# Kernel optimization log

Measured on AMD Instinct MI355X. Metric: run time of the kernel, lower is better.

Reference implementation:

```python
import jax, jax.numpy as jnp
import numpy as np

EPS = 1e-12  # torch F.normalize clamp_min eps


def _linear_interp(t, M):
    # PyTorch F.interpolate(mode='linear', align_corners=False) along last axis.
    L = t.shape[-1]
    src = (jnp.arange(M, dtype=t.dtype) + 0.5) * (L / M) - 0.5
    src = jnp.maximum(src, 0.0)
    i0 = jnp.minimum(jnp.floor(src).astype(jnp.int32), L - 1)
    i1 = jnp.minimum(i0 + 1, L - 1)
    frac = src - i0.astype(t.dtype)
    return t[..., i0] * (1.0 - frac) + t[..., i1] * frac


def _l2norm(t):
    n = jnp.linalg.norm(t, axis=-1, keepdims=True)
    return t / jnp.maximum(n, EPS)


def setup_inputs() -> dict:
    key = jax.random.key(0)
    ks = jax.random.split(key, 6)
    b, dim, m = 4, 512, 4096
    h = w = 64
    heads = 8
    s = 0.02
    return {
        "x": jax.random.normal(ks[0], (b, dim, m), dtype=jnp.float32),
        "y": jax.random.normal(ks[1], (b, dim, h, w), dtype=jnp.float32),
        "temperature": jnp.ones((heads, 1, 1), dtype=jnp.float32),
        "w_kv": jax.random.normal(ks[2], (2 * dim, dim), dtype=jnp.float32) * s,
        "w_q": jax.random.normal(ks[3], (dim, dim), dtype=jnp.float32) * s,
        "w_dw": jax.random.normal(ks[4], (dim, dim, 3, 3), dtype=jnp.float32) * s,
        "w_out": jax.random.normal(ks[5], (dim, dim), dtype=jnp.float32) * s,
    }


def reference(x, y, temperature, w_kv, w_q, w_dw, w_out):
    b, c, m = x.shape
    heads = temperature.shape[0]
    hd = c // heads

    # kv = Conv1d(dim, 2*dim, k=1)(x); split into k, v
    kv = jnp.einsum('bcm,oc->bom', x, w_kv)
    k, v = jnp.split(kv, 2, axis=1)

    # q = dwconv3x3(Conv2d 1x1(y)) -> flatten -> linear-resize to m
    q = jnp.einsum('bchw,oc->bohw', y, w_q)
    q = jax.lax.conv_general_dilated(
        q, w_dw, window_strides=(1, 1), padding=[(1, 1), (1, 1)],
        dimension_numbers=('NCHW', 'OIHW', 'NCHW'))
    q = q.reshape(b, c, -1)
    q = _linear_interp(q, m)

    # split heads: [b, head, c', m]
    q = _l2norm(q.reshape(b, heads, hd, m))
    k = _l2norm(k.reshape(b, heads, hd, m))
    v = v.reshape(b, heads, hd, m)

    # channel-wise attention: [b, head, c', c']
    attn = jnp.einsum('bhcm,bhdm->bhcd', q, k) * temperature
    attn = jax.nn.softmax(attn, axis=-1)
    out = jnp.einsum('bhcd,bhdm->bhcm', attn, v).reshape(b, c, m)

    # project_out: Conv1d k=1
    return jnp.einsum('bcm,oc->bom', out, w_out)
```

## Files before the change

kernel.cpp:

```cpp
#include <hip/hip_runtime.h>
#include <hip/hip_bf16.h>
#include <math.h>

typedef float f32x4 __attribute__((ext_vector_type(4)));
typedef int   i32x4 __attribute__((ext_vector_type(4)));
typedef short s16x8 __attribute__((ext_vector_type(8)));

#define NB 4
#define NC 512
#define NM 4096
#define NHEADS 8

#define GLDS16(src, dst) __builtin_amdgcn_global_load_lds( \
    (const __attribute__((address_space(1))) void*)(src),  \
    (__attribute__((address_space(3))) void*)(dst), 16, 0, 0)

__global__ __launch_bounds__(256) void prep(
    const float* __restrict__ wdw, const float* __restrict__ wkv,
    const float* __restrict__ wq,
    __hip_bfloat16* __restrict__ Wr, __hip_bfloat16* __restrict__ wkvB,
    __hip_bfloat16* __restrict__ wqT, __hip_bfloat16* __restrict__ zeropad,
    float* __restrict__ norms)
{
  long idx = (long)blockIdx.x * 256 + threadIdx.x;
  if (idx < 2359296) {
    int r = (int)(idx / 262144);
    int rem = (int)(idx % 262144);
    int o = rem >> 9, i = rem & 511;
    Wr[idx] = __float2bfloat16(wdw[((long)o * 512 + i) * 9 + r]);
  } else if (idx < 2883584) {
    long j = idx - 2359296;
    wkvB[j] = __float2bfloat16(wkv[j]);
  } else if (idx < 3145728) {
    long j = idx - 2883584;
    int c = (int)(j >> 9), cp = (int)(j & 511);
    wqT[j] = __float2bfloat16(wq[(long)cp * 512 + c]);
  } else if (idx < 3145856) {
    zeropad[idx - 3145728] = __float2bfloat16(0.f);
  } else if (idx < 3149952) {
    norms[idx - 3145856] = 0.f;
  }
}

__global__ __launch_bounds__(256) void transpose_k(
    const float* __restrict__ x, const float* __restrict__ y,
    __hip_bfloat16* __restrict__ xT, __hip_bfloat16* __restrict__ yT)
{
  __shared__ __hip_bfloat16 tile[64][68];
  int z = blockIdx.z;
  const float* src = ((z < 4) ? x : y) + (long)(z & 3) * ((long)NC * NM);
  __hip_bfloat16* dst = (z < 4 ? xT : yT) + (long)(z & 3) * ((long)NC * NM);
  int tm = blockIdx.x * 64, tc = blockIdx.y * 64;
  int tx4 = threadIdx.x & 15, trow = threadIdx.x >> 4;
  #pragma unroll
  for (int p = 0; p < 4; p++) {
    int crow = trow + p * 16;
    f32x4 v = *(const f32x4*)&src[(long)(tc + crow) * NM + tm + tx4 * 4];
    #pragma unroll
    for (int t = 0; t < 4; t++) tile[crow][tx4 * 4 + t] = __float2bfloat16(v[t]);
  }
  __syncthreads();
  #pragma unroll
  for (int p = 0; p < 4; p++) {
    int mrow = trow + p * 16;
    union { ushort4 u4; unsigned short u[4]; } o;
    #pragma unroll
    for (int t = 0; t < 4; t++)
      o.u[t] = *(const unsigned short*)&tile[tx4 * 4 + t][mrow];
    *(ushort4*)&dst[(long)(tm + mrow) * NC + tc + tx4 * 4] = o.u4;
  }
}

__global__ __launch_bounds__(256) void gemm_bt(
    const __hip_bfloat16* __restrict__ Aall, long sA,
    const __hip_bfloat16* __restrict__ Ball, long sB,
    __hip_bfloat16* __restrict__ Cball, float* __restrict__ Cfall, long sC,
    int M, int N, int Kd, int outF32)
{
  const __hip_bfloat16* A = Aall + (long)blockIdx.z * sA;
  const __hip_bfloat16* B = Ball + (long)blockIdx.z * sB;
  const int m0 = blockIdx.y * 128, n0 = blockIdx.x * 128;
  __shared__ __hip_bfloat16 As[128 * 32];
  __shared__ __hip_bfloat16 Bs[128 * 32];
  const int tid = threadIdx.x;
  const int wid = tid >> 6, lane = tid & 63;
  const int wm = (wid >> 1) * 64, wn = (wid & 1) * 64;
  const int quad = lane >> 4, l16 = lane & 15;
  const int srow = wid * 32 + (lane >> 2);
  const int scol = (lane & 3) * 8;
  f32x4 acc[4][4] = {};
  for (int k0 = 0; k0 < Kd; k0 += 32) {
    __syncthreads();
    #pragma unroll
    for (int t = 0; t < 2; t++) {
      GLDS16(A + (long)(m0 + srow + t * 16) * Kd + k0 + scol,
             As + (wid * 32 + t * 16) * 32);
      GLDS16(B + (long)(n0 + srow + t * 16) * Kd + k0 + scol,
             Bs + (wid * 32 + t * 16) * 32);
    }
    __builtin_amdgcn_s_waitcnt(0);
    __syncthreads();
    s16x8 bfr[4];
    #pragma unroll
    for (int j = 0; j < 4; j++)
      bfr[j] = *(const s16x8*)(&Bs[(wn + j * 16 + l16) * 32 + quad * 8]);
    #pragma unroll
    for (int i = 0; i < 4; i++) {
      s16x8 af = *(const s16x8*)(&As[(wm + i * 16 + l16) * 32 + quad * 8]);
      #pragma unroll
      for (int j = 0; j < 4; j++)
        acc[i][j] = __builtin_amdgcn_mfma_f32_16x16x32_bf16(af, bfr[j], acc[i][j], 0, 0, 0);
    }
  }
  if (outF32) {
    float* C = Cfall + (long)blockIdx.z * sC;
    #pragma unroll
    for (int i = 0; i < 4; i++)
      #pragma unroll
      for (int j = 0; j < 4; j++) {
        int rbase = m0 + wm + i * 16 + quad * 4;
        int col = n0 + wn + j * 16 + l16;
        #pragma unroll
        for (int r = 0; r < 4; r++)
          C[(long)(rbase + r) * N + col] = acc[i][j][r];
      }
  } else {
    __hip_bfloat16* C = Cball + (long)blockIdx.z * sC;
    #pragma unroll
    for (int i = 0; i < 4; i++)
      #pragma unroll
      for (int j = 0; j < 4; j++) {
        int rbase = m0 + wm + i * 16 + quad * 4;
        int col = n0 + wn + j * 16 + l16;
        #pragma unroll
        for (int r = 0; r < 4; r++)
          C[(long)(rbase + r) * N + col] = __float2bfloat16(acc[i][j][r]);
      }
  }
}

__global__ __launch_bounds__(256) void gemm_kv(
    const __hip_bfloat16* __restrict__ wkvB,
    const __hip_bfloat16* __restrict__ xT,
    __hip_bfloat16* __restrict__ Kb,
    __hip_bfloat16* __restrict__ Vt,
    float* __restrict__ knorm2)
{
  const int z = blockIdx.z;
  const int b = z & 3;
  const bool kmode = (z < 4);
  const long S = (long)NM * NC;
  const __hip_bfloat16* A = kmode ? wkvB : (xT + b * S);
  const __hip_bfloat16* B = kmode ? (xT + b * S) : (wkvB + 262144);
  __hip_bfloat16* C = kmode ? (Kb + b * S) : (Vt + b * S);
  const int m0 = (kmode ? blockIdx.y : blockIdx.x) * 128;
  const int n0 = (kmode ? blockIdx.x : blockIdx.y) * 128;
  const int N = kmode ? NM : NC;
  __shared__ __hip_bfloat16 As[128 * 32];
  __shared__ __hip_bfloat16 Bs[128 * 32];
  const int tid = threadIdx.x;
  const int wid = tid >> 6, lane = tid & 63;
  const int wm = (wid >> 1) * 64, wn = (wid & 1) * 64;
  const int quad = lane >> 4, l16 = lane & 15;
  const int srow = wid * 32 + (lane >> 2);
  const int scol = (lane & 3) * 8;
  f32x4 acc[4][4] = {};
  for (int k0 = 0; k0 < NC; k0 += 32) {
    __syncthreads();
    #pragma unroll
    for (int t = 0; t < 2; t++) {
      GLDS16(A + (long)(m0 + srow + t * 16) * NC + k0 + scol,
             As + (wid * 32 + t * 16) * 32);
      GLDS16(B + (long)(n0 + srow + t * 16) * NC + k0 + scol,
             Bs + (wid * 32 + t * 16) * 32);
    }
    __builtin_amdgcn_s_waitcnt(0);
    __syncthreads();
    s16x8 bfr[4];
    #pragma unroll
    for (int j = 0; j < 4; j++)
      bfr[j] = *(const s16x8*)(&Bs[(wn + j * 16 + l16) * 32 + quad * 8]);
    #pragma unroll
    for (int i = 0; i < 4; i++) {
      s16x8 af = *(const s16x8*)(&As[(wm + i * 16 + l16) * 32 + quad * 8]);
      #pragma unroll
      for (int j = 0; j < 4; j++)
        acc[i][j] = __builtin_amdgcn_mfma_f32_16x16x32_bf16(af, bfr[j], acc[i][j], 0, 0, 0);
    }
  }
  #pragma unroll
  for (int i = 0; i < 4; i++)
    #pragma unroll
    for (int j = 0; j < 4; j++) {
      int rbase = m0 + wm + i * 16 + quad * 4;
      int col = n0 + wn + j * 16 + l16;
      #pragma unroll
      for (int r = 0; r < 4; r++)
        C[(long)(rbase + r) * N + col] = __float2bfloat16(acc[i][j][r]);
    }
  if (kmode) {
    #pragma unroll
    for (int i = 0; i < 4; i++) {
      int rbase = m0 + wm + i * 16 + quad * 4;
      #pragma unroll
      for (int r = 0; r < 4; r++) {
        float s = 0.f;
        #pragma unroll
        for (int j = 0; j < 4; j++) s += acc[i][j][r] * acc[i][j][r];
        s += __shfl_xor(s, 1); s += __shfl_xor(s, 2);
        s += __shfl_xor(s, 4); s += __shfl_xor(s, 8);
        if (l16 == 0) atomicAdd(&knorm2[b * 512 + rbase + r], s);
      }
    }
  }
}

__global__ __launch_bounds__(256) void conv3x3(
    const __hip_bfloat16* __restrict__ Wt,
    const __hip_bfloat16* __restrict__ yT,
    const __hip_bfloat16* __restrict__ zeropad,
    __hip_bfloat16* __restrict__ q2,
    float* __restrict__ qnorm2)
{
  const int b = blockIdx.z;
  const int n0 = blockIdx.x * 128;
  const int m0 = blockIdx.y * 128;
  __shared__ __hip_bfloat16 As3[3 * 128 * 32];
  __shared__ __hip_bfloat16 Bs[256 * 32];
  const int tid = threadIdx.x;
  const int wid = tid >> 6, lane = tid & 63;
  const int wm = (wid >> 1) * 64, wn = (wid & 1) * 64;
  const int quad = lane >> 4, l16 = lane & 15;
  const int lrow = lane >> 2, scol = (lane & 3) * 8;
  const int h0 = n0 >> 6;
  const __hip_bfloat16* yb = yT + (long)b * NM * NC;
  f32x4 acc[4][4] = {};
  const s16x8 zero8 = {0, 0, 0, 0, 0, 0, 0, 0};

  for (int ic = 0; ic < 512; ic += 32) {
    #pragma unroll
    for (int g = 0; g < 3; g++) {
      __syncthreads();
      if (g == 0) {
        #pragma unroll
        for (int t = 0; t < 4; t++) {
          int p = wid * 64 + t * 16 + lrow;
          int hw = (h0 - 1) * 64 + p;
          const __hip_bfloat16* src = (((unsigned)hw) < (unsigned)NM)
              ? (yb + (long)hw * NC + ic + scol) : (zeropad + scol % 8);
          GLDS16(src, Bs + (wid * 64 + t * 16) * 32);
        }
      }
      #pragma unroll
      for (int t = 0; t < 3; t++) {
        int r = g * 3 + t;
        #pragma unroll
        for (int t2 = 0; t2 < 2; t2++) {
          GLDS16(Wt + ((long)r * 512 + m0 + wid * 32 + t2 * 16 + lrow) * 512 + ic + scol,
                 As3 + (t * 128 + wid * 32 + t2 * 16) * 32);
        }
      }
      __builtin_amdgcn_s_waitcnt(0);
      __syncthreads();
      const int dy = g - 1;
      #pragma unroll
      for (int t = 0; t < 3; t++) {
        const int dx = t - 1;
        s16x8 bfr[4];
        #pragma unroll
        for (int j = 0; j < 4; j++) {
          int nl = wn + j * 16 + l16;
          int wq_ = nl & 63, hr = nl >> 6;
          int wp = wq_ + dx;
          bool v = ((unsigned)wp) < 64u;
          int p = v ? ((hr + 1 + dy) * 64 + wp) : 0;
          s16x8 tt = *(const s16x8*)(&Bs[p * 32 + quad * 8]);
          bfr[j] = v ? tt : zero8;
        }
        #pragma unroll
        for (int i = 0; i < 4; i++) {
          s16x8 af = *(const s16x8*)(&As3[(t * 128 + wm + i * 16 + l16) * 32 + quad * 8]);
          #pragma unroll
          for (int j = 0; j < 4; j++)
            acc[i][j] = __builtin_amdgcn_mfma_f32_16x16x32_bf16(af, bfr[j], acc[i][j], 0, 0, 0);
        }
      }
    }
  }
  __hip_bfloat16* Cb = q2 + (long)b * NC * NM;
  #pragma unroll
  for (int i = 0; i < 4; i++)
    #pragma unroll
    for (int j = 0; j < 4; j++) {
      int rbase = m0 + wm + i * 16 + quad * 4;
      int col = n0 + wn + j * 16 + l16;
      #pragma unroll
      for (int r = 0; r < 4; r++)
        Cb[(long)(rbase + r) * NM + col] = __float2bfloat16(acc[i][j][r]);
    }
  #pragma unroll
  for (int i = 0; i < 4; i++) {
    int rbase = m0 + wm + i * 16 + quad * 4;
    #pragma unroll
    for (int r = 0; r < 4; r++) {
      float s = 0.f;
      #pragma unroll
      for (int j = 0; j < 4; j++) s += acc[i][j][r] * acc[i][j][r];
      s += __shfl_xor(s, 1); s += __shfl_xor(s, 2);
      s += __shfl_xor(s, 4); s += __shfl_xor(s, 8);
      if (l16 == 0) atomicAdd(&qnorm2[b * 512 + rbase + r], s);
    }
  }
}

__global__ __launch_bounds__(256) void attn_g(
    const __hip_bfloat16* __restrict__ q2, const __hip_bfloat16* __restrict__ Kb,
    float* __restrict__ Gpart)
{
  const int mc = blockIdx.x, h = blockIdx.y, b = blockIdx.z;
  const __hip_bfloat16* qrow = q2 + ((long)b * NC + h * 64) * NM + mc * 512;
  const __hip_bfloat16* krow = Kb + ((long)b * NC + h * 64) * NM + mc * 512;
  __shared__ __hip_bfloat16 Qs[64 * 40];
  __shared__ __hip_bfloat16 Ks[64 * 40];
  const int tid = threadIdx.x;
  const int wid = tid >> 6, lane = tid & 63;
  const int wc = (wid >> 1) * 32, wd = (wid & 1) * 32;
  const int quad = lane >> 4, l16 = lane & 15;
  const int srow = tid >> 2, scol = (tid & 3) * 8;
  f32x4 acc[2][2] = {};
  for (int k0 = 0; k0 < 512; k0 += 32) {
    __syncthreads();
    *(i32x4*)(&Qs[srow * 40 + scol]) = *(const i32x4*)(&qrow[(long)srow * NM + k0 + scol]);
    *(i32x4*)(&Ks[srow * 40 + scol]) = *(const i32x4*)(&krow[(long)srow * NM + k0 + scol]);
    __syncthreads();
    s16x8 bfr[2];
    #pragma unroll
    for (int j = 0; j < 2; j++)
      bfr[j] = *(const s16x8*)(&Ks[(wd + j * 16 + l16) * 40 + quad * 8]);
    #pragma unroll
    for (int i = 0; i < 2; i++) {
      s16x8 af = *(const s16x8*)(&Qs[(wc + i * 16 + l16) * 40 + quad * 8]);
      #pragma unroll
      for (int j = 0; j < 2; j++)
        acc[i][j] = __builtin_amdgcn_mfma_f32_16x16x32_bf16(af, bfr[j], acc[i][j], 0, 0, 0);
    }
  }
  float* gp = Gpart + ((long)((b * 8 + h) * 8 + mc)) * 4096;
  #pragma unroll
  for (int i = 0; i < 2; i++)
    #pragma unroll
    for (int j = 0; j < 2; j++)
      #pragma unroll
      for (int r = 0; r < 4; r++)
        gp[(wc + i * 16 + quad * 4 + r) * 64 + wd + j * 16 + l16] = acc[i][j][r];
}

__global__ __launch_bounds__(256) void softmax_wa(
    const float* __restrict__ Gpart, const float* __restrict__ qnorm2,
    const float* __restrict__ knorm2, const float* __restrict__ temp,
    const float* __restrict__ wout, __hip_bfloat16* __restrict__ Wa)
{
  const int oc = blockIdx.x, h = blockIdx.y, b = blockIdx.z;
  __shared__ float G[64][64];
  __shared__ float Wt[64][65];
  const int tid = threadIdx.x;
  const float tv = temp[h];
  for (int e = tid; e < 4096; e += 256) {
    float s = 0.f;
    #pragma unroll
    for (int p = 0; p < 8; p++)
      s += Gpart[((long)((b * 8 + h) * 8 + p)) * 4096 + e];
    int c = e >> 6, d = e & 63;
    float qn = fmaxf(sqrtf(qnorm2[b * 512 + h * 64 + c]), 1e-12f);
    float kn = fmaxf(sqrtf(knorm2[b * 512 + h * 64 + d]), 1e-12f);
    G[c][d] = s * tv / (qn * kn);
    Wt[c][d] = wout[(long)(oc * 64 + c) * 512 + h * 64 + d];
  }
  __syncthreads();
  int row = tid >> 2, s4 = tid & 3;
  float mx = -1e30f;
  for (int d = s4; d < 64; d += 4) mx = fmaxf(mx, G[row][d]);
  mx = fmaxf(mx, __shfl_xor(mx, 1));
  mx = fmaxf(mx, __shfl_xor(mx, 2));
  float sum = 0.f;
  for (int d = s4; d < 64; d += 4) { float e = __expf(G[row][d] - mx); G[row][d] = e; sum += e; }
  sum += __shfl_xor(sum, 1);
  sum += __shfl_xor(sum, 2);
  float inv = 1.f / sum;
  for (int d = s4; d < 64; d += 4) G[row][d] *= inv;
  __syncthreads();
  int d = tid & 63, og = tid >> 6;
  #pragma unroll
  for (int k2 = 0; k2 < 16; k2++) {
    int o = og * 16 + k2;
    float s = 0.f;
    #pragma unroll 8
    for (int c = 0; c < 64; c++) s += Wt[o][c] * G[c][d];
    Wa[((long)b * 512 + oc * 64 + o) * 512 + h * 64 + d] = __float2bfloat16(s);
  }
}

extern "C" void kernel_launch(void* const* d_in, const int* in_sizes, int n_in,
                              void* d_out, int out_size, void* d_ws, size_t ws_size,
                              hipStream_t stream) {
  const float* x    = (const float*)d_in[0];
  const float* y    = (const float*)d_in[1];
  const float* temp = (const float*)d_in[2];
  const float* wkv  = (const float*)d_in[3];
  const float* wq   = (const float*)d_in[4];
  const float* wdw  = (const float*)d_in[5];
  const float* wout = (const float*)d_in[6];
  float* out = (float*)d_out;

  char* ws = (char*)d_ws;
  const long TEN = 16777216;
  __hip_bfloat16* xT  = (__hip_bfloat16*)(ws);
  __hip_bfloat16* q2  = xT;
  __hip_bfloat16* yT  = (__hip_bfloat16*)(ws + TEN);
  float* Gpart        = (float*)(ws + TEN);
  __hip_bfloat16* Wa  = (__hip_bfloat16*)(ws + TEN + 4718592);
  __hip_bfloat16* Kb  = (__hip_bfloat16*)(ws + 2 * TEN);
  __hip_bfloat16* Vt  = (__hip_bfloat16*)(ws + 3 * TEN);
  __hip_bfloat16* Wfold = (__hip_bfloat16*)(ws + 4 * TEN);
  __hip_bfloat16* Wr    = (__hip_bfloat16*)(ws + 4 * TEN + 4718592);
  __hip_bfloat16* wkvB  = (__hip_bfloat16*)(ws + 4 * TEN + 9437184);
  __hip_bfloat16* wqT   = (__hip_bfloat16*)(ws + 4 * TEN + 10485760);
  __hip_bfloat16* zeropad = (__hip_bfloat16*)(ws + 4 * TEN + 11010048);
  float* norms          = (float*)(ws + 4 * TEN + 11010304);
  float* knorm2 = norms;
  float* qnorm2 = norms + 2048;

  const long S = (long)4096 * 512;
  const long S2 = (long)512 * 512;
  dim3 blk(256);

  prep<<<dim3(12305), blk, 0, stream>>>(wdw, wkv, wq, Wr, wkvB, wqT, zeropad, norms);
  transpose_k<<<dim3(64, 8, 8), blk, 0, stream>>>(x, y, xT, yT);
  gemm_bt<<<dim3(4, 4, 9), blk, 0, stream>>>(Wr, S2, wqT, 0L, Wfold, nullptr, S2, 512, 512, 512, 0);
  gemm_kv<<<dim3(32, 4, 8), blk, 0, stream>>>(wkvB, xT, Kb, Vt, knorm2);
  conv3x3<<<dim3(32, 4, 4), blk, 0, stream>>>(Wfold, yT, zeropad, q2, qnorm2);
  attn_g<<<dim3(8, 8, 4), blk, 0, stream>>>(q2, Kb, Gpart);
  softmax_wa<<<dim3(8, 8, 4), blk, 0, stream>>>(Gpart, qnorm2, knorm2, temp, wout, Wa);
  gemm_bt<<<dim3(32, 4, 4), blk, 0, stream>>>(Wa, S2, Vt, S, nullptr, out, S, 512, 4096, 512, 1);
  (void)in_sizes; (void)n_in; (void)out_size; (void)ws_size;
}
```

Baseline: 307.3 us.

## Load conv weights directly from global, swizzle LDS tile, precompute B addresses

The 3x3 conv GEMM kernel no longer stages the weight tile in LDS. Each wave now reads its A fragments straight from global memory, so only the input halo tile goes through LDS, with one barrier pair per channel chunk instead of three. The halo tile gets an XOR swizzle to cut LDS bank conflicts, and the per-tap B addresses and validity bits are computed once outside the loop. The trade-off is that A fragments now come from global or cache inside the MFMA loop with no staging, which can expose memory latency.

```diff
diff --git a/kernel.cpp b/kernel.cpp
--- a/kernel.cpp
+++ b/kernel.cpp
@@ -225,61 +225,62 @@
   const int b = blockIdx.z;
   const int n0 = blockIdx.x * 128;
   const int m0 = blockIdx.y * 128;
-  __shared__ __hip_bfloat16 As3[3 * 128 * 32];
   __shared__ __hip_bfloat16 Bs[256 * 32];
   const int tid = threadIdx.x;
   const int wid = tid >> 6, lane = tid & 63;
   const int wm = (wid >> 1) * 64, wn = (wid & 1) * 64;
   const int quad = lane >> 4, l16 = lane & 15;
-  const int lrow = lane >> 2, scol = (lane & 3) * 8;
+  const int lrow = lane >> 2;
   const int h0 = n0 >> 6;
   const __hip_bfloat16* yb = yT + (long)b * NM * NC;
   f32x4 acc[4][4] = {};
   const s16x8 zero8 = {0, 0, 0, 0, 0, 0, 0, 0};
 
+  const int sq = ((lane & 3) ^ ((lane >> 3) & 3)) * 8;
+
+  const __hip_bfloat16* Abase = Wt + ((long)(m0 + wm + l16) * 512) + quad * 8;
+
+  int addr0[3][4];
+  unsigned vbits = 0;
+  #pragma unroll
+  for (int t = 0; t < 3; t++) {
+    #pragma unroll
+    for (int j = 0; j < 4; j++) {
+      int nl = wn + j * 16 + l16;
+      int wq_ = nl & 63, hr = nl >> 6;
+      int wp = wq_ + t - 1;
+      unsigned v = ((unsigned)wp) < 64u;
+      int p = v ? (hr * 64 + wp) : 0;
+      addr0[t][j] = p * 32 + ((quad ^ ((p >> 1) & 3)) * 8);
+      vbits |= v << (t * 4 + j);
+    }
+  }
+
   for (int ic = 0; ic < 512; ic += 32) {
+    __syncthreads();
+    #pragma unroll
+    for (int t = 0; t < 4; t++) {
+      int p = wid * 64 + t * 16 + lrow;
+      int hw = (h0 - 1) * 64 + p;
+      const __hip_bfloat16* src = (((unsigned)hw) < (unsigned)NM)
+          ? (yb + (long)hw * NC + ic + sq) : zeropad;
+      GLDS16(src, Bs + (wid * 64 + t * 16) * 32);
+    }
+    __builtin_amdgcn_s_waitcnt(0);
+    __syncthreads();
     #pragma unroll
     for (int g = 0; g < 3; g++) {
-      __syncthreads();
-      if (g == 0) {
-        #pragma unroll
-        for (int t = 0; t < 4; t++) {
-          int p = wid * 64 + t * 16 + lrow;
-          int hw = (h0 - 1) * 64 + p;
-          const __hip_bfloat16* src = (((unsigned)hw) < (unsigned)NM)
-              ? (yb + (long)hw * NC + ic + scol) : (zeropad + scol % 8);
-          GLDS16(src, Bs + (wid * 64 + t * 16) * 32);
-        }
-      }
       #pragma unroll
       for (int t = 0; t < 3; t++) {
-        int r = g * 3 + t;
-        #pragma unroll
-        for (int t2 = 0; t2 < 2; t2++) {
-          GLDS16(Wt + ((long)r * 512 + m0 + wid * 32 + t2 * 16 + lrow) * 512 + ic + scol,
-                 As3 + (t * 128 + wid * 32 + t2 * 16) * 32);
-        }
-      }
-      __builtin_amdgcn_s_waitcnt(0);
-      __syncthreads();
-      const int dy = g - 1;
-      #pragma unroll
-      for (int t = 0; t < 3; t++) {
-        const int dx = t - 1;
         s16x8 bfr[4];
         #pragma unroll
         for (int j = 0; j < 4; j++) {
-          int nl = wn + j * 16 + l16;
-          int wq_ = nl & 63, hr = nl >> 6;
-          int wp = wq_ + dx;
-          bool v = ((unsigned)wp) < 64u;
-          int p = v ? ((hr + 1 + dy) * 64 + wp) : 0;
-          s16x8 tt = *(const s16x8*)(&Bs[p * 32 + quad * 8]);
-          bfr[j] = v ? tt : zero8;
+          s16x8 tt = *(const s16x8*)(&Bs[addr0[t][j] + g * 2048]);
+          bfr[j] = ((vbits >> (t * 4 + j)) & 1u) ? tt : zero8;
         }
         #pragma unroll
         for (int i = 0; i < 4; i++) {
-          s16x8 af = *(const s16x8*)(&As3[(t * 128 + wm + i * 16 + l16) * 32 + quad * 8]);
+          s16x8 af = *(const s16x8*)(Abase + (long)((g * 3 + t) * 262144 + i * 8192 + ic));
           #pragma unroll
           for (int j = 0; j < 4; j++)
             acc[i][j] = __builtin_amdgcn_mfma_f32_16x16x32_bf16(af, bfr[j], acc[i][j], 0, 0, 0);
```

Measured after the change: 373.4 us. 1.22x slower.
